# Kernel tuning notes

Measured on AMD Instinct MI355X. Metric: run time of the kernel, lower is better.

The kernel has to match this reference:

```python
import jax, jax.numpy as jnp
import numpy as np

B, S, E, H = 32, 4096, 1024, 16
D = E // H  # head_dim = 64


def setup_inputs() -> dict:
    key = jax.random.key(0)
    ks = jax.random.split(key, 6)
    scale = 1.0 / np.sqrt(E)
    x = jax.random.normal(ks[0], (B, S, E), dtype=jnp.float32)
    mask = jax.random.randint(ks[1], (B, S), 0, 2).astype(bool)  # True = masked key
    in_proj_w = jax.random.uniform(ks[2], (3 * E, E), jnp.float32, -scale, scale)
    in_proj_b = jnp.zeros((3 * E,), jnp.float32)
    out_w = jax.random.uniform(ks[3], (E, E), jnp.float32, -scale, scale)
    out_b = jnp.zeros((E,), jnp.float32)
    return {"x": x, "mask": mask, "in_proj_w": in_proj_w, "in_proj_b": in_proj_b,
            "out_w": out_w, "out_b": out_b}


def reference(x, mask, in_proj_w, in_proj_b, out_w, out_b):
    # nn.MultiheadAttention with q = x[:, 0:1, :], k = v = x, key_padding_mask=mask
    Wq, Wk, Wv = in_proj_w[:E], in_proj_w[E:2 * E], in_proj_w[2 * E:]
    bq, bk, bv = in_proj_b[:E], in_proj_b[E:2 * E], in_proj_b[2 * E:]
    q = (x[:, 0, :] @ Wq.T + bq).reshape(B, H, D)            # (B,H,D)
    k = (x @ Wk.T + bk).reshape(B, S, H, D)                  # (B,S,H,D)
    v = (x @ Wv.T + bv).reshape(B, S, H, D)
    scores = jnp.einsum('bhd,bshd->bhs', q, k) / np.sqrt(D)  # (B,H,S)
    scores = jnp.where(mask[:, None, :], jnp.float32(-1e30), scores)
    attn = jax.nn.softmax(scores, axis=-1)                   # (B,H,S)
    ctx = jnp.einsum('bhs,bshd->bhd', attn, v).reshape(B, E)
    out = ctx @ out_w.T + out_b                              # (B,E) == attn_output.squeeze(1)
    attn_weights = attn.mean(axis=1)[:, None, :]             # (B,1,S): heads averaged
    return out, attn_weights
```

## Files before the change

### kernel.cpp

```cpp
#include <hip/hip_runtime.h>
#include <math.h>


constexpr int cB = 32, cS = 4096, cE = 1024, cH = 16, cD = 64, cNC = 16;

constexpr size_t OFF_P    = 0;
constexpr size_t OFF_C    = OFF_P + 524288;
constexpr size_t OFF_Q    = OFF_C + 512;
constexpr size_t OFF_SC   = OFF_Q + 32768;
constexpr size_t OFF_CTX  = OFF_SC + 2097152;
constexpr size_t OFF_SM   = OFF_CTX + 32768;
constexpr size_t OFF_SL   = OFF_SM + 8192;
constexpr size_t OFF_MF   = OFF_SL + 8192;
constexpr size_t OFF_IL   = OFF_MF + 512;
constexpr size_t OFF_PART = OFF_IL + 512;

__device__ inline float wave_max64(float v) {
#pragma unroll
  for (int m = 1; m < 64; m <<= 1) v = fmaxf(v, __shfl_xor(v, m));
  return v;
}
__device__ inline float wave_sum64(float v) {
#pragma unroll
  for (int m = 1; m < 64; m <<= 1) v += __shfl_xor(v, m);
  return v;
}

__global__ __launch_bounds__(256) void k1a_q(const float* __restrict__ x,
                                             const float* __restrict__ w,
                                             const float* __restrict__ bias,
                                             float* __restrict__ q) {
  int b = blockIdx.x >> 3, blk = blockIdx.x & 7;
  int tid = threadIdx.x;
  __shared__ float x0[cE];
  ((float4*)x0)[tid] = ((const float4*)(x + (size_t)b * cS * cE))[tid];
  __syncthreads();
  int row = blk * 128 + (tid >> 1);
  int half = tid & 1;
  const float* wr = w + (size_t)row * cE + half * 512;
  const float* xl = x0 + half * 512;
  float acc = 0.f;
#pragma unroll 4
  for (int j = 0; j < 128; ++j) {
    float4 a = *(const float4*)(wr + j * 4);
    float4 xv = *(const float4*)(xl + j * 4);
    acc = fmaf(a.x, xv.x, acc); acc = fmaf(a.y, xv.y, acc);
    acc = fmaf(a.z, xv.z, acc); acc = fmaf(a.w, xv.w, acc);
  }
  float tot = acc + __shfl_xor(acc, 1);
  if (!half) q[b * cE + row] = tot + bias[row];
}

__global__ __launch_bounds__(256) void k1b_p(const float* __restrict__ w,
                                             const float* __restrict__ bvec,
                                             const float* __restrict__ q,
                                             float* __restrict__ p,
                                             float* __restrict__ cb) {
  int b = blockIdx.x >> 3, sub = blockIdx.x & 7;
  int ec = sub >> 1, hh = sub & 1;
  int tid = threadIdx.x;
  int e = ec * 256 + tid;
  __shared__ float ql[cE];
  ((float4*)ql)[tid] = ((const float4*)(q + (size_t)b * cE))[tid];
  __syncthreads();
  for (int hi = 0; hi < 8; ++hi) {
    int h = hh * 8 + hi;
    float acc = 0.f;
    const float* wb = w + (size_t)(cE + h * cD) * cE + e;
    const float* qh = ql + h * cD;
#pragma unroll 8
    for (int d = 0; d < cD; ++d) acc = fmaf(wb[(size_t)d * cE], qh[d], acc);
    p[(size_t)(b * cH + h) * cE + e] = 0.125f * acc;
  }
  if (ec == 0 && tid < 8) {
    int h = hh * 8 + tid;
    float cacc = 0.f;
    for (int d = 0; d < cD; ++d) cacc = fmaf(ql[h * cD + d], bvec[cE + h * cD + d], cacc);
    cb[b * cH + h] = 0.125f * cacc;
  }
}

__global__ __launch_bounds__(256) void k2_scores(const float* __restrict__ x,
                                                 const float* __restrict__ p,
                                                 const float* __restrict__ cbias,
                                                 const int* __restrict__ mask,
                                                 float* __restrict__ scores,
                                                 float* __restrict__ statsM,
                                                 float* __restrict__ statsL) {
  __shared__ float xT[2][32 * 256];
  int bx = blockIdx.x;
  int b = bx >> 4, sc = bx & 15;
  int s_base = sc * 256;
  int tid = threadIdx.x;
  int s_t = tid & 63, h_t = tid >> 6;
  int h0 = __builtin_amdgcn_readfirstlane(h_t * 4);
  float acc[4][4];
#pragma unroll
  for (int i = 0; i < 4; ++i)
#pragma unroll
    for (int j = 0; j < 4; ++j) acc[i][j] = 0.f;

  const float* xb = x + ((size_t)b * cS + s_base) * cE;
  const float* __restrict__ pu = p + (size_t)(b * cH + h0) * cE;

  float4 sv[8];
  int r_ = tid >> 3, c4_ = tid & 7;

#pragma unroll
  for (int i = 0; i < 8; ++i)
    sv[i] = *(const float4*)(xb + (size_t)(i * 32 + r_) * cE + c4_ * 4);
  {
    float* xd = xT[0];
#pragma unroll
    for (int i = 0; i < 8; ++i) {
      int r = i * 32 + r_;
      float vv[4] = {sv[i].x, sv[i].y, sv[i].z, sv[i].w};
#pragma unroll
      for (int j = 0; j < 4; ++j) {
        int e = c4_ * 4 + j;
        int f = (e ^ (e >> 4)) & 15;
        xd[e * 256 + ((((r >> 2) ^ f) << 2) | (r & 3))] = vv[j];
      }
    }
  }
  __syncthreads();

  for (int kt = 1; kt <= 32; ++kt) {
    if (kt < 32) {
#pragma unroll
      for (int i = 0; i < 8; ++i)
        sv[i] = *(const float4*)(xb + (size_t)(i * 32 + r_) * cE + kt * 32 + c4_ * 4);
    }
    {
      const float* xs = xT[(kt - 1) & 1];
      const int kb = (kt - 1) * 32;
#pragma unroll 8
      for (int e = 0; e < 32; ++e) {
        int f = (e ^ (e >> 4)) & 15;
        float4 xv = *(const float4*)&xs[e * 256 + ((s_t ^ f) << 2)];
        float p0 = pu[kb + e];
        float p1 = pu[cE + kb + e];
        float p2 = pu[2 * cE + kb + e];
        float p3 = pu[3 * cE + kb + e];
        float xa[4] = {xv.x, xv.y, xv.z, xv.w};
        float pa[4] = {p0, p1, p2, p3};
#pragma unroll
        for (int si = 0; si < 4; ++si)
#pragma unroll
          for (int hj = 0; hj < 4; ++hj) acc[si][hj] = fmaf(xa[si], pa[hj], acc[si][hj]);
      }
    }
    if (kt < 32) {
      float* xd = xT[kt & 1];
#pragma unroll
      for (int i = 0; i < 8; ++i) {
        int r = i * 32 + r_;
        float vv[4] = {sv[i].x, sv[i].y, sv[i].z, sv[i].w};
#pragma unroll
        for (int j = 0; j < 4; ++j) {
          int e = c4_ * 4 + j;
          int f = (e ^ (e >> 4)) & 15;
          xd[e * 256 + ((((r >> 2) ^ f) << 2) | (r & 3))] = vv[j];
        }
      }
    }
    __syncthreads();
  }

  float4 cv = *(const float4*)(cbias + b * cH + h0);
  float ca[4] = {cv.x, cv.y, cv.z, cv.w};
  int4 m4 = *(const int4*)(mask + (size_t)b * cS + s_base + s_t * 4);
#pragma unroll
  for (int hj = 0; hj < 4; ++hj) {
    float v0 = m4.x ? -1e30f : acc[0][hj] + ca[hj];
    float v1 = m4.y ? -1e30f : acc[1][hj] + ca[hj];
    float v2 = m4.z ? -1e30f : acc[2][hj] + ca[hj];
    float v3 = m4.w ? -1e30f : acc[3][hj] + ca[hj];
    *(float4*)(scores + (size_t)(b * cH + h0 + hj) * cS + s_base + s_t * 4) =
        make_float4(v0, v1, v2, v3);
    float mx = fmaxf(fmaxf(v0, v1), fmaxf(v2, v3));
    float wm = wave_max64(mx);
    float es = __expf(v0 - wm) + __expf(v1 - wm) + __expf(v2 - wm) + __expf(v3 - wm);
    float wsum = wave_sum64(es);
    if (s_t == 0) {
      statsM[(size_t)(b * cH + h0 + hj) * cNC + sc] = wm;
      statsL[(size_t)(b * cH + h0 + hj) * cNC + sc] = wsum;
    }
  }
}

__global__ __launch_bounds__(64) void k3t_stats(const float* __restrict__ statsM,
                                                const float* __restrict__ statsL,
                                                float* __restrict__ Mf,
                                                float* __restrict__ iLf) {
  int bh = blockIdx.x * 64 + threadIdx.x;
  const float* sm = statsM + (size_t)bh * cNC;
  const float* sl = statsL + (size_t)bh * cNC;
  float M = -3e38f;
#pragma unroll
  for (int c = 0; c < cNC; ++c) M = fmaxf(M, sm[c]);
  float L = 0.f;
#pragma unroll
  for (int c = 0; c < cNC; ++c) L += sl[c] * __expf(sm[c] - M);
  Mf[bh] = M;
  iLf[bh] = 1.0f / L;
}

__global__ __launch_bounds__(256) void k4_wsum(const float* __restrict__ x,
                                               const float* __restrict__ scores,
                                               const float* __restrict__ Mf,
                                               const float* __restrict__ iLf,
                                               float* __restrict__ part,
                                               float* __restrict__ out) {
  __shared__ float al[2][cH][64];
  int bx = blockIdx.x;
  int b = bx >> 4, sc = bx & 15;
  int tid = threadIdx.x;
  int wv = tid >> 6, lane = tid & 63;
  int e0 = tid * 4;
  const float* xb = x + ((size_t)b * cS + sc * 256) * cE + e0;
  const float* sb = scores + (size_t)b * cH * cS + sc * 256;

  float4 acc[16];
#pragma unroll
  for (int h = 0; h < cH; ++h) acc[h] = make_float4(0.f, 0.f, 0.f, 0.f);

#pragma unroll
  for (int j = 0; j < 4; ++j) {
    int h = wv * 4 + j;
    float Mh = Mf[b * cH + h];
    float iLh = iLf[b * cH + h];
    float v = sb[(size_t)h * cS + lane];
    al[0][h][lane] = __expf(v - Mh) * iLh;
  }
  __syncthreads();

  for (int g = 0; g < 4; ++g) {
    if (g < 3) {
#pragma unroll
      for (int j = 0; j < 4; ++j) {
        int h = wv * 4 + j;
        float Mh = Mf[b * cH + h];
        float iLh = iLf[b * cH + h];
        float v = sb[(size_t)h * cS + (g + 1) * 64 + lane];
        al[(g + 1) & 1][h][lane] = __expf(v - Mh) * iLh;
      }
    }
    const float (*ab)[64] = al[g & 1];
    const float* xg = xb + (size_t)(g * 64) * cE;
#pragma unroll 4
    for (int s = 0; s < 64; ++s) {
      float4 xv = *(const float4*)(xg + (size_t)s * cE);
      float aa[16];
#pragma unroll
      for (int h = 0; h < cH; ++h) aa[h] = ab[h][s];
#pragma unroll
      for (int h = 0; h < cH; ++h) {
        acc[h].x = fmaf(aa[h], xv.x, acc[h].x);
        acc[h].y = fmaf(aa[h], xv.y, acc[h].y);
        acc[h].z = fmaf(aa[h], xv.z, acc[h].z);
        acc[h].w = fmaf(aa[h], xv.w, acc[h].w);
      }
    }
    if (wv == g) {
      float ms = 0.f;
#pragma unroll
      for (int h = 0; h < cH; ++h) ms += ab[h][lane];
      out[cB * cE + (size_t)b * cS + sc * 256 + g * 64 + lane] = ms * (1.0f / 16.0f);
    }
    __syncthreads();
  }

  float* pb = part + ((size_t)(b * cNC + sc) * cH) * cE + e0;
#pragma unroll
  for (int h = 0; h < cH; ++h) *(float4*)(pb + (size_t)h * cE) = acc[h];
}

__global__ __launch_bounds__(256) void k5_ctx(const float* __restrict__ w,
                                              const float* __restrict__ bvec,
                                              const float* __restrict__ part,
                                              float* __restrict__ ctx) {
  int b = blockIdx.x >> 4, h = blockIdx.x & 15;
  int tid = threadIdx.x;
  __shared__ float yl[cE];
  float4 a = make_float4(0.f, 0.f, 0.f, 0.f);
  const float* pb = part + ((size_t)(b * cNC) * cH + h) * cE + tid * 4;
#pragma unroll
  for (int s = 0; s < cNC; ++s) {
    float4 v = *(const float4*)(pb + (size_t)s * cH * cE);
    a.x += v.x; a.y += v.y; a.z += v.z; a.w += v.w;
  }
  *(float4*)(yl + tid * 4) = a;
  __syncthreads();
  int wid = tid >> 6, lane = tid & 63;
  for (int i = 0; i < 16; ++i) {
    int d = wid * 16 + i;
    const float* wr = w + (size_t)(2 * cE + h * cD + d) * cE + lane * 16;
    const float* yr = yl + lane * 16;
    float partial = 0.f;
#pragma unroll
    for (int j = 0; j < 4; ++j) {
      float4 wvv = *(const float4*)(wr + j * 4);
      float4 yv = *(const float4*)(yr + j * 4);
      partial = fmaf(wvv.x, yv.x, partial); partial = fmaf(wvv.y, yv.y, partial);
      partial = fmaf(wvv.z, yv.z, partial); partial = fmaf(wvv.w, yv.w, partial);
    }
    partial = wave_sum64(partial);
    if (lane == 0) ctx[b * cE + h * cD + d] = partial + bvec[2 * cE + h * cD + d];
  }
}

__global__ __launch_bounds__(256) void k6_out(const float* __restrict__ w,
                                              const float* __restrict__ bvec,
                                              const float* __restrict__ ctx,
                                              float* __restrict__ out) {
  int b = blockIdx.x >> 3, br = blockIdx.x & 7;
  int tid = threadIdx.x;
  __shared__ float cl[cE];
  ((float4*)cl)[tid] = ((const float4*)(ctx + (size_t)b * cE))[tid];
  __syncthreads();
  int wid = tid >> 6, lane = tid & 63;
  for (int i = 0; i < 32; ++i) {
    int row = br * 128 + wid * 32 + i;
    const float* wr = w + (size_t)row * cE + lane * 16;
    const float* cr = cl + lane * 16;
    float partial = 0.f;
#pragma unroll
    for (int j = 0; j < 4; ++j) {
      float4 wvv = *(const float4*)(wr + j * 4);
      float4 cvv = *(const float4*)(cr + j * 4);
      partial = fmaf(wvv.x, cvv.x, partial); partial = fmaf(wvv.y, cvv.y, partial);
      partial = fmaf(wvv.z, cvv.z, partial); partial = fmaf(wvv.w, cvv.w, partial);
    }
    partial = wave_sum64(partial);
    if (lane == 0) out[(size_t)b * cE + row] = partial + bvec[row];
  }
}

extern "C" void kernel_launch(void* const* d_in, const int* in_sizes, int n_in,
                              void* d_out, int out_size, void* d_ws, size_t ws_size,
                              hipStream_t stream) {
  const float* x = (const float*)d_in[0];
  const int* mask = (const int*)d_in[1];
  const float* in_proj_w = (const float*)d_in[2];
  const float* in_proj_b = (const float*)d_in[3];
  const float* out_w = (const float*)d_in[4];
  const float* out_b = (const float*)d_in[5];
  float* out = (float*)d_out;
  float* W = (float*)d_ws;

  float* p = W + OFF_P;
  float* cb = W + OFF_C;
  float* q = W + OFF_Q;
  float* scores = W + OFF_SC;
  float* ctx = W + OFF_CTX;
  float* statsM = W + OFF_SM;
  float* statsL = W + OFF_SL;
  float* Mf = W + OFF_MF;
  float* iLf = W + OFF_IL;
  float* part = W + OFF_PART;

  k1a_q<<<256, 256, 0, stream>>>(x, in_proj_w, in_proj_b, q);
  k1b_p<<<256, 256, 0, stream>>>(in_proj_w, in_proj_b, q, p, cb);
  k2_scores<<<512, 256, 0, stream>>>(x, p, cb, mask, scores, statsM, statsL);
  k3t_stats<<<8, 64, 0, stream>>>(statsM, statsL, Mf, iLf);
  k4_wsum<<<512, 256, 0, stream>>>(x, scores, Mf, iLf, part, out);
  k5_ctx<<<512, 256, 0, stream>>>(in_proj_w, in_proj_b, part, ctx);
  k6_out<<<256, 256, 0, stream>>>(out_w, out_b, ctx, out);
}
```

Before: 374.8 us.

## Fuse score computation and weighted V-sum into one online-softmax kernel

Merges the score, stats and weighted-sum kernels into a single pass over x using a running max and sum (flash-style online softmax), so x is read from HBM once instead of twice. Per-chunk partial sums are rescaled and combined in the context kernel, and the head-averaged attention weights move to a separate small kernel that rereads the stored scores. The fused kernel launches only 256 blocks with 256 threads and about 128KB of LDS, so occupancy is low and there are many barriers per 16-row step. Its score dot-product loop also issues a long serial chain of LDS reads.

After: 663.9 us. +77.1%, slower.

```diff
diff --git a/kernel.cpp b/kernel.cpp
--- a/kernel.cpp
+++ b/kernel.cpp
@@ -2,24 +2,21 @@
 #include <math.h>
 
 
-constexpr int cB = 32, cS = 4096, cE = 1024, cH = 16, cD = 64, cNC = 16;
+constexpr int cB = 32, cS = 4096, cE = 1024, cH = 16, cD = 64;
+constexpr int cCK = 8;
+constexpr int cSUB = 32;
 
 constexpr size_t OFF_P    = 0;
 constexpr size_t OFF_C    = OFF_P + 524288;
 constexpr size_t OFF_Q    = OFF_C + 512;
 constexpr size_t OFF_SC   = OFF_Q + 32768;
-constexpr size_t OFF_CTX  = OFF_SC + 2097152;
-constexpr size_t OFF_SM   = OFF_CTX + 32768;
-constexpr size_t OFF_SL   = OFF_SM + 8192;
-constexpr size_t OFF_MF   = OFF_SL + 8192;
+constexpr size_t OFF_SM   = OFF_SC + 2097152;
+constexpr size_t OFF_SL   = OFF_SM + 4096;
+constexpr size_t OFF_MF   = OFF_SL + 4096;
 constexpr size_t OFF_IL   = OFF_MF + 512;
-constexpr size_t OFF_PART = OFF_IL + 512;
-
-__device__ inline float wave_max64(float v) {
-#pragma unroll
-  for (int m = 1; m < 64; m <<= 1) v = fmaxf(v, __shfl_xor(v, m));
-  return v;
-}
+constexpr size_t OFF_CTX  = OFF_IL + 512;
+constexpr size_t OFF_PART = OFF_CTX + 32768;
+
 __device__ inline float wave_sum64(float v) {
 #pragma unroll
   for (int m = 1; m < 64; m <<= 1) v += __shfl_xor(v, m);
@@ -80,180 +77,118 @@
   }
 }
 
-__global__ __launch_bounds__(256) void k2_scores(const float* __restrict__ x,
-                                                 const float* __restrict__ p,
-                                                 const float* __restrict__ cbias,
-                                                 const int* __restrict__ mask,
-                                                 float* __restrict__ scores,
-                                                 float* __restrict__ statsM,
-                                                 float* __restrict__ statsL) {
-  __shared__ float xT[2][32 * 256];
-  int bx = blockIdx.x;
-  int b = bx >> 4, sc = bx & 15;
-  int s_base = sc * 256;
-  int tid = threadIdx.x;
-  int s_t = tid & 63, h_t = tid >> 6;
-  int h0 = __builtin_amdgcn_readfirstlane(h_t * 4);
-  float acc[4][4];
-#pragma unroll
-  for (int i = 0; i < 4; ++i)
-#pragma unroll
-    for (int j = 0; j < 4; ++j) acc[i][j] = 0.f;
-
-  const float* xb = x + ((size_t)b * cS + s_base) * cE;
-  const float* __restrict__ pu = p + (size_t)(b * cH + h0) * cE;
-
-  float4 sv[8];
-  int r_ = tid >> 3, c4_ = tid & 7;
-
-#pragma unroll
-  for (int i = 0; i < 8; ++i)
-    sv[i] = *(const float4*)(xb + (size_t)(i * 32 + r_) * cE + c4_ * 4);
-  {
-    float* xd = xT[0];
-#pragma unroll
-    for (int i = 0; i < 8; ++i) {
-      int r = i * 32 + r_;
-      float vv[4] = {sv[i].x, sv[i].y, sv[i].z, sv[i].w};
-#pragma unroll
-      for (int j = 0; j < 4; ++j) {
-        int e = c4_ * 4 + j;
-        int f = (e ^ (e >> 4)) & 15;
-        xd[e * 256 + ((((r >> 2) ^ f) << 2) | (r & 3))] = vv[j];
-      }
-    }
-  }
-  __syncthreads();
-
-  for (int kt = 1; kt <= 32; ++kt) {
-    if (kt < 32) {
-#pragma unroll
-      for (int i = 0; i < 8; ++i)
-        sv[i] = *(const float4*)(xb + (size_t)(i * 32 + r_) * cE + kt * 32 + c4_ * 4);
-    }
-    {
-      const float* xs = xT[(kt - 1) & 1];
-      const int kb = (kt - 1) * 32;
+__global__ __launch_bounds__(256, 1) void kfuse(const float* __restrict__ x,
+                                                const float* __restrict__ p,
+                                                const float* __restrict__ cb,
+                                                const int* __restrict__ mask,
+                                                float* __restrict__ scores,
+                                                float* __restrict__ statsM,
+                                                float* __restrict__ statsL,
+                                                float* __restrict__ part) {
+  __shared__ __align__(16) float pl[cH * cE];
+  __shared__ __align__(16) float xt[16 * cE];
+  __shared__ __align__(16) float exb[16 * cH];
+  __shared__ __align__(16) float scl[cH];
+  int b = blockIdx.x >> 3, ck = blockIdx.x & 7;
+  int tid = threadIdx.x;
+  int sA = tid & 15, hA = tid >> 4;
+  int s0g = ck * 512;
+
+#pragma unroll
+  for (int j = 0; j < 16; ++j) {
+    int idx4 = j * 256 + tid;
+    ((float4*)pl)[idx4] =
+        *(const float4*)(p + (size_t)(b * cH + (idx4 >> 8)) * cE + (size_t)(idx4 & 255) * 4);
+  }
+  float cbh = cb[b * cH + hA];
+
+  float4 acc[16];
+#pragma unroll
+  for (int h = 0; h < cH; ++h) acc[h] = make_float4(0.f, 0.f, 0.f, 0.f);
+  float m_run = -1e30f, l_run = 0.f;
+
+  const float* xbase = x + ((size_t)b * cS + s0g + (tid >> 4)) * cE + (size_t)(tid & 15) * 4;
+  int sw = tid >> 4;
+  int e4b = tid & 15;
+  float4 rv[16];
+#pragma unroll
+  for (int j = 0; j < 16; ++j) rv[j] = *(const float4*)(xbase + j * 64);
+  __syncthreads();
+
+  float4* xt4 = (float4*)xt;
+  const float4* ph4 = (const float4*)(pl + hA * cE);
+  const float4* exb4 = (const float4*)exb;
+  const float4* scl4 = (const float4*)scl;
+
+  for (int sub = 0; sub < cSUB; ++sub) {
+#pragma unroll
+    for (int j = 0; j < 16; ++j) {
+      int e4 = e4b + 16 * j;
+      xt4[sw * 256 + (e4 ^ sw)] = rv[j];
+    }
+    if (sub < cSUB - 1) {
+      const float* xn = xbase + (size_t)(sub + 1) * 16 * cE;
+#pragma unroll
+      for (int j = 0; j < 16; ++j) rv[j] = *(const float4*)(xn + j * 64);
+    }
+    __syncthreads();
+
+    float d0 = 0.f, d1 = 0.f, d2 = 0.f, d3 = 0.f;
 #pragma unroll 8
-      for (int e = 0; e < 32; ++e) {
-        int f = (e ^ (e >> 4)) & 15;
-        float4 xv = *(const float4*)&xs[e * 256 + ((s_t ^ f) << 2)];
-        float p0 = pu[kb + e];
-        float p1 = pu[cE + kb + e];
-        float p2 = pu[2 * cE + kb + e];
-        float p3 = pu[3 * cE + kb + e];
-        float xa[4] = {xv.x, xv.y, xv.z, xv.w};
-        float pa[4] = {p0, p1, p2, p3};
-#pragma unroll
-        for (int si = 0; si < 4; ++si)
-#pragma unroll
-          for (int hj = 0; hj < 4; ++hj) acc[si][hj] = fmaf(xa[si], pa[hj], acc[si][hj]);
-      }
-    }
-    if (kt < 32) {
-      float* xd = xT[kt & 1];
-#pragma unroll
-      for (int i = 0; i < 8; ++i) {
-        int r = i * 32 + r_;
-        float vv[4] = {sv[i].x, sv[i].y, sv[i].z, sv[i].w};
-#pragma unroll
-        for (int j = 0; j < 4; ++j) {
-          int e = c4_ * 4 + j;
-          int f = (e ^ (e >> 4)) & 15;
-          xd[e * 256 + ((((r >> 2) ^ f) << 2) | (r & 3))] = vv[j];
-        }
-      }
-    }
+    for (int e4 = 0; e4 < 256; e4 += 4) {
+      float4 x0 = xt4[sA * 256 + ((e4 + 0) ^ sA)];
+      float4 p0 = ph4[e4 + 0];
+      d0 = fmaf(x0.x, p0.x, d0); d0 = fmaf(x0.y, p0.y, d0);
+      d0 = fmaf(x0.z, p0.z, d0); d0 = fmaf(x0.w, p0.w, d0);
+      float4 x1 = xt4[sA * 256 + ((e4 + 1) ^ sA)];
+      float4 p1 = ph4[e4 + 1];
+      d1 = fmaf(x1.x, p1.x, d1); d1 = fmaf(x1.y, p1.y, d1);
+      d1 = fmaf(x1.z, p1.z, d1); d1 = fmaf(x1.w, p1.w, d1);
+      float4 x2 = xt4[sA * 256 + ((e4 + 2) ^ sA)];
+      float4 p2 = ph4[e4 + 2];
+      d2 = fmaf(x2.x, p2.x, d2); d2 = fmaf(x2.y, p2.y, d2);
+      d2 = fmaf(x2.z, p2.z, d2); d2 = fmaf(x2.w, p2.w, d2);
+      float4 x3 = xt4[sA * 256 + ((e4 + 3) ^ sA)];
+      float4 p3 = ph4[e4 + 3];
+      d3 = fmaf(x3.x, p3.x, d3); d3 = fmaf(x3.y, p3.y, d3);
+      d3 = fmaf(x3.z, p3.z, d3); d3 = fmaf(x3.w, p3.w, d3);
+    }
+    float score = (d0 + d1) + (d2 + d3) + cbh;
+    int sg = s0g + sub * 16 + sA;
+    if (mask[(size_t)b * cS + sg]) score = -1e30f;
+    scores[(size_t)(b * cH + hA) * cS + sg] = score;
+    float gm = score;
+#pragma unroll
+    for (int m = 1; m < 16; m <<= 1) gm = fmaxf(gm, __shfl_xor(gm, m));
+    float mnew = fmaxf(m_run, gm);
+    float rs = __expf(m_run - mnew);
+    float ex = __expf(score - mnew);
+    float gs = ex;
+#pragma unroll
+    for (int m = 1; m < 16; m <<= 1) gs += __shfl_xor(gs, m);
+    l_run = l_run * rs + gs;
+    m_run = mnew;
+    exb[sA * cH + hA] = ex;
+    if (sA == 0) scl[hA] = rs;
     __syncthreads();
-  }
-
-  float4 cv = *(const float4*)(cbias + b * cH + h0);
-  float ca[4] = {cv.x, cv.y, cv.z, cv.w};
-  int4 m4 = *(const int4*)(mask + (size_t)b * cS + s_base + s_t * 4);
-#pragma unroll
-  for (int hj = 0; hj < 4; ++hj) {
-    float v0 = m4.x ? -1e30f : acc[0][hj] + ca[hj];
-    float v1 = m4.y ? -1e30f : acc[1][hj] + ca[hj];
-    float v2 = m4.z ? -1e30f : acc[2][hj] + ca[hj];
-    float v3 = m4.w ? -1e30f : acc[3][hj] + ca[hj];
-    *(float4*)(scores + (size_t)(b * cH + h0 + hj) * cS + s_base + s_t * 4) =
-        make_float4(v0, v1, v2, v3);
-    float mx = fmaxf(fmaxf(v0, v1), fmaxf(v2, v3));
-    float wm = wave_max64(mx);
-    float es = __expf(v0 - wm) + __expf(v1 - wm) + __expf(v2 - wm) + __expf(v3 - wm);
-    float wsum = wave_sum64(es);
-    if (s_t == 0) {
-      statsM[(size_t)(b * cH + h0 + hj) * cNC + sc] = wm;
-      statsL[(size_t)(b * cH + h0 + hj) * cNC + sc] = wsum;
-    }
-  }
-}
-
-__global__ __launch_bounds__(64) void k3t_stats(const float* __restrict__ statsM,
-                                                const float* __restrict__ statsL,
-                                                float* __restrict__ Mf,
-                                                float* __restrict__ iLf) {
-  int bh = blockIdx.x * 64 + threadIdx.x;
-  const float* sm = statsM + (size_t)bh * cNC;
-  const float* sl = statsL + (size_t)bh * cNC;
-  float M = -3e38f;
-#pragma unroll
-  for (int c = 0; c < cNC; ++c) M = fmaxf(M, sm[c]);
-  float L = 0.f;
-#pragma unroll
-  for (int c = 0; c < cNC; ++c) L += sl[c] * __expf(sm[c] - M);
-  Mf[bh] = M;
-  iLf[bh] = 1.0f / L;
-}
-
-__global__ __launch_bounds__(256) void k4_wsum(const float* __restrict__ x,
-                                               const float* __restrict__ scores,
-                                               const float* __restrict__ Mf,
-                                               const float* __restrict__ iLf,
-                                               float* __restrict__ part,
-                                               float* __restrict__ out) {
-  __shared__ float al[2][cH][64];
-  int bx = blockIdx.x;
-  int b = bx >> 4, sc = bx & 15;
-  int tid = threadIdx.x;
-  int wv = tid >> 6, lane = tid & 63;
-  int e0 = tid * 4;
-  const float* xb = x + ((size_t)b * cS + sc * 256) * cE + e0;
-  const float* sb = scores + (size_t)b * cH * cS + sc * 256;
-
-  float4 acc[16];
-#pragma unroll
-  for (int h = 0; h < cH; ++h) acc[h] = make_float4(0.f, 0.f, 0.f, 0.f);
-
-#pragma unroll
-  for (int j = 0; j < 4; ++j) {
-    int h = wv * 4 + j;
-    float Mh = Mf[b * cH + h];
-    float iLh = iLf[b * cH + h];
-    float v = sb[(size_t)h * cS + lane];
-    al[0][h][lane] = __expf(v - Mh) * iLh;
-  }
-  __syncthreads();
-
-  for (int g = 0; g < 4; ++g) {
-    if (g < 3) {
-#pragma unroll
-      for (int j = 0; j < 4; ++j) {
-        int h = wv * 4 + j;
-        float Mh = Mf[b * cH + h];
-        float iLh = iLf[b * cH + h];
-        float v = sb[(size_t)h * cS + (g + 1) * 64 + lane];
-        al[(g + 1) & 1][h][lane] = __expf(v - Mh) * iLh;
-      }
-    }
-    const float (*ab)[64] = al[g & 1];
-    const float* xg = xb + (size_t)(g * 64) * cE;
+
+#pragma unroll
+    for (int k = 0; k < 4; ++k) {
+      float4 sv = scl4[k];
+      acc[k * 4 + 0].x *= sv.x; acc[k * 4 + 0].y *= sv.x; acc[k * 4 + 0].z *= sv.x; acc[k * 4 + 0].w *= sv.x;
+      acc[k * 4 + 1].x *= sv.y; acc[k * 4 + 1].y *= sv.y; acc[k * 4 + 1].z *= sv.y; acc[k * 4 + 1].w *= sv.y;
+      acc[k * 4 + 2].x *= sv.z; acc[k * 4 + 2].y *= sv.z; acc[k * 4 + 2].z *= sv.z; acc[k * 4 + 2].w *= sv.z;
+      acc[k * 4 + 3].x *= sv.w; acc[k * 4 + 3].y *= sv.w; acc[k * 4 + 3].z *= sv.w; acc[k * 4 + 3].w *= sv.w;
+    }
 #pragma unroll 4
-    for (int s = 0; s < 64; ++s) {
-      float4 xv = *(const float4*)(xg + (size_t)s * cE);
-      float aa[16];
-#pragma unroll
-      for (int h = 0; h < cH; ++h) aa[h] = ab[h][s];
+    for (int s = 0; s < 16; ++s) {
+      float4 xv = xt4[s * 256 + (tid ^ s)];
+      float4 ea = exb4[s * 4 + 0];
+      float4 eb = exb4[s * 4 + 1];
+      float4 ec = exb4[s * 4 + 2];
+      float4 ed = exb4[s * 4 + 3];
+      float aa[16] = {ea.x, ea.y, ea.z, ea.w, eb.x, eb.y, eb.z, eb.w,
+                      ec.x, ec.y, ec.z, ec.w, ed.x, ed.y, ed.z, ed.w};
 #pragma unroll
       for (int h = 0; h < cH; ++h) {
         acc[h].x = fmaf(aa[h], xv.x, acc[h].x);
@@ -262,34 +197,51 @@
         acc[h].w = fmaf(aa[h], xv.w, acc[h].w);
       }
     }
-    if (wv == g) {
-      float ms = 0.f;
-#pragma unroll
-      for (int h = 0; h < cH; ++h) ms += ab[h][lane];
-      out[cB * cE + (size_t)b * cS + sc * 256 + g * 64 + lane] = ms * (1.0f / 16.0f);
-    }
     __syncthreads();
   }
 
-  float* pb = part + ((size_t)(b * cNC + sc) * cH) * cE + e0;
+  float* pb = part + (size_t)(b * cCK + ck) * cH * cE + (size_t)tid * 4;
 #pragma unroll
   for (int h = 0; h < cH; ++h) *(float4*)(pb + (size_t)h * cE) = acc[h];
+  if (sA == 0) {
+    statsM[(b * cH + hA) * cCK + ck] = m_run;
+    statsL[(b * cH + hA) * cCK + ck] = l_run;
+  }
 }
 
 __global__ __launch_bounds__(256) void k5_ctx(const float* __restrict__ w,
                                               const float* __restrict__ bvec,
                                               const float* __restrict__ part,
-                                              float* __restrict__ ctx) {
+                                              const float* __restrict__ statsM,
+                                              const float* __restrict__ statsL,
+                                              float* __restrict__ ctx,
+                                              float* __restrict__ Mf,
+                                              float* __restrict__ iLf) {
   int b = blockIdx.x >> 4, h = blockIdx.x & 15;
+  int bh = b * cH + h;
   int tid = threadIdx.x;
   __shared__ float yl[cE];
+  float M = -3e38f;
+#pragma unroll
+  for (int c = 0; c < cCK; ++c) M = fmaxf(M, statsM[bh * cCK + c]);
+  float L = 0.f;
+  float wgt[cCK];
+#pragma unroll
+  for (int c = 0; c < cCK; ++c) {
+    wgt[c] = __expf(statsM[bh * cCK + c] - M);
+    L += statsL[bh * cCK + c] * wgt[c];
+  }
+  float iL = 1.0f / L;
+  if (blockIdx.x < 512 && tid == 0) { Mf[bh] = M; iLf[bh] = iL; }
   float4 a = make_float4(0.f, 0.f, 0.f, 0.f);
-  const float* pb = part + ((size_t)(b * cNC) * cH + h) * cE + tid * 4;
-#pragma unroll
-  for (int s = 0; s < cNC; ++s) {
-    float4 v = *(const float4*)(pb + (size_t)s * cH * cE);
-    a.x += v.x; a.y += v.y; a.z += v.z; a.w += v.w;
-  }
+  const float* pb = part + (size_t)b * cCK * cH * cE + (size_t)h * cE + (size_t)tid * 4;
+#pragma unroll
+  for (int c = 0; c < cCK; ++c) {
+    float4 v = *(const float4*)(pb + (size_t)c * cH * cE);
+    a.x = fmaf(v.x, wgt[c], a.x); a.y = fmaf(v.y, wgt[c], a.y);
+    a.z = fmaf(v.z, wgt[c], a.z); a.w = fmaf(v.w, wgt[c], a.w);
+  }
+  a.x *= iL; a.y *= iL; a.z *= iL; a.w *= iL;
   *(float4*)(yl + tid * 4) = a;
   __syncthreads();
   int wid = tid >> 6, lane = tid & 63;
@@ -300,14 +252,29 @@
     float partial = 0.f;
 #pragma unroll
     for (int j = 0; j < 4; ++j) {
-      float4 wvv = *(const float4*)(wr + j * 4);
+      float4 wv = *(const float4*)(wr + j * 4);
       float4 yv = *(const float4*)(yr + j * 4);
-      partial = fmaf(wvv.x, yv.x, partial); partial = fmaf(wvv.y, yv.y, partial);
-      partial = fmaf(wvv.z, yv.z, partial); partial = fmaf(wvv.w, yv.w, partial);
+      partial = fmaf(wv.x, yv.x, partial); partial = fmaf(wv.y, yv.y, partial);
+      partial = fmaf(wv.z, yv.z, partial); partial = fmaf(wv.w, yv.w, partial);
     }
     partial = wave_sum64(partial);
     if (lane == 0) ctx[b * cE + h * cD + d] = partial + bvec[2 * cE + h * cD + d];
   }
+}
+
+__global__ __launch_bounds__(256) void kmean(const float* __restrict__ scores,
+                                             const float* __restrict__ Mf,
+                                             const float* __restrict__ iLf,
+                                             float* __restrict__ out) {
+  int idx = blockIdx.x * 256 + threadIdx.x;
+  int b = idx >> 12, s = idx & 4095;
+  float sum = 0.f;
+#pragma unroll
+  for (int h = 0; h < cH; ++h) {
+    float v = scores[(size_t)(b * cH + h) * cS + s];
+    sum += __expf(v - Mf[b * cH + h]) * iLf[b * cH + h];
+  }
+  out[cB * cE + (size_t)b * cS + s] = sum * (1.0f / 16.0f);
 }
 
 __global__ __launch_bounds__(256) void k6_out(const float* __restrict__ w,
@@ -327,10 +294,10 @@
     float partial = 0.f;
 #pragma unroll
     for (int j = 0; j < 4; ++j) {
-      float4 wvv = *(const float4*)(wr + j * 4);
-      float4 cvv = *(const float4*)(cr + j * 4);
-      partial = fmaf(wvv.x, cvv.x, partial); partial = fmaf(wvv.y, cvv.y, partial);
-      partial = fmaf(wvv.z, cvv.z, partial); partial = fmaf(wvv.w, cvv.w, partial);
+      float4 wv = *(const float4*)(wr + j * 4);
+      float4 cv = *(const float4*)(cr + j * 4);
+      partial = fmaf(wv.x, cv.x, partial); partial = fmaf(wv.y, cv.y, partial);
+      partial = fmaf(wv.z, cv.z, partial); partial = fmaf(wv.w, cv.w, partial);
     }
     partial = wave_sum64(partial);
     if (lane == 0) out[(size_t)b * cE + row] = partial + bvec[row];
@@ -353,18 +320,17 @@
   float* cb = W + OFF_C;
   float* q = W + OFF_Q;
   float* scores = W + OFF_SC;
-  float* ctx = W + OFF_CTX;
   float* statsM = W + OFF_SM;
   float* statsL = W + OFF_SL;
   float* Mf = W + OFF_MF;
   float* iLf = W + OFF_IL;
+  float* ctx = W + OFF_CTX;
   float* part = W + OFF_PART;
 
   k1a_q<<<256, 256, 0, stream>>>(x, in_proj_w, in_proj_b, q);
   k1b_p<<<256, 256, 0, stream>>>(in_proj_w, in_proj_b, q, p, cb);
-  k2_scores<<<512, 256, 0, stream>>>(x, p, cb, mask, scores, statsM, statsL);
-  k3t_stats<<<8, 64, 0, stream>>>(statsM, statsL, Mf, iLf);
-  k4_wsum<<<512, 256, 0, stream>>>(x, scores, Mf, iLf, part, out);
-  k5_ctx<<<512, 256, 0, stream>>>(in_proj_w, in_proj_b, part, ctx);
+  kfuse<<<256, 256, 0, stream>>>(x, p, cb, mask, scores, statsM, statsL, part);
+  k5_ctx<<<512, 256, 0, stream>>>(in_proj_w, in_proj_b, part, statsM, statsL, ctx, Mf, iLf);
+  kmean<<<512, 256, 0, stream>>>(scores, Mf, iLf, out);
   k6_out<<<256, 256, 0, stream>>>(out_w, out_b, ctx, out);
 }
```

## Transpose attention weight tile in wsum and batch four rows per Wv block

Applied to the files above, without the earlier changes.

In the weighted-sum kernel the shared softmax-weight tile becomes [s][h] with padding, so each step reads 16 head weights as four float4 loads instead of 16 scalar loads. Per-head max and inverse sum are hoisted out of the loop. The context kernel now processes four batch rows per block, so each Wv row is read once for four batches, with 128 blocks instead of 512. The per-thread full dot product drops the wave reductions but gives fewer blocks, which may lower occupancy.

New measurement: 412.8 us. 10.2% more time.

```diff
diff --git a/kernel.cpp b/kernel.cpp
--- a/kernel.cpp
+++ b/kernel.cpp
@@ -8,12 +8,12 @@
 constexpr size_t OFF_C    = OFF_P + 524288;
 constexpr size_t OFF_Q    = OFF_C + 512;
 constexpr size_t OFF_SC   = OFF_Q + 32768;
-constexpr size_t OFF_CTX  = OFF_SC + 2097152;
-constexpr size_t OFF_SM   = OFF_CTX + 32768;
+constexpr size_t OFF_SM   = OFF_SC + 2097152;
 constexpr size_t OFF_SL   = OFF_SM + 8192;
 constexpr size_t OFF_MF   = OFF_SL + 8192;
 constexpr size_t OFF_IL   = OFF_MF + 512;
-constexpr size_t OFF_PART = OFF_IL + 512;
+constexpr size_t OFF_CTX  = OFF_IL + 512;
+constexpr size_t OFF_PART = OFF_CTX + 32768;
 
 __device__ inline float wave_max64(float v) {
 #pragma unroll
@@ -212,48 +212,49 @@
                                                const float* __restrict__ iLf,
                                                float* __restrict__ part,
                                                float* __restrict__ out) {
-  __shared__ float al[2][cH][64];
+  __shared__ float al[2][64][20];
   int bx = blockIdx.x;
   int b = bx >> 4, sc = bx & 15;
   int tid = threadIdx.x;
   int wv = tid >> 6, lane = tid & 63;
   int e0 = tid * 4;
-  const float* xb = x + ((size_t)b * cS + sc * 256) * cE + e0;
   const float* sb = scores + (size_t)b * cH * cS + sc * 256;
-
+  int h0w = wv * 4;
+  float M4[4], iL4[4];
+#pragma unroll
+  for (int j = 0; j < 4; ++j) {
+    M4[j] = Mf[b * cH + h0w + j];
+    iL4[j] = iLf[b * cH + h0w + j];
+  }
   float4 acc[16];
 #pragma unroll
   for (int h = 0; h < cH; ++h) acc[h] = make_float4(0.f, 0.f, 0.f, 0.f);
 
 #pragma unroll
   for (int j = 0; j < 4; ++j) {
-    int h = wv * 4 + j;
-    float Mh = Mf[b * cH + h];
-    float iLh = iLf[b * cH + h];
-    float v = sb[(size_t)h * cS + lane];
-    al[0][h][lane] = __expf(v - Mh) * iLh;
-  }
-  __syncthreads();
-
+    float v = sb[(size_t)(h0w + j) * cS + lane];
+    al[0][lane][h0w + j] = __expf(v - M4[j]) * iL4[j];
+  }
+  __syncthreads();
+
+  const float* xg = x + ((size_t)b * cS + sc * 256) * cE + e0;
   for (int g = 0; g < 4; ++g) {
+    int buf = g & 1;
     if (g < 3) {
 #pragma unroll
       for (int j = 0; j < 4; ++j) {
-        int h = wv * 4 + j;
-        float Mh = Mf[b * cH + h];
-        float iLh = iLf[b * cH + h];
-        float v = sb[(size_t)h * cS + (g + 1) * 64 + lane];
-        al[(g + 1) & 1][h][lane] = __expf(v - Mh) * iLh;
-      }
-    }
-    const float (*ab)[64] = al[g & 1];
-    const float* xg = xb + (size_t)(g * 64) * cE;
+        float v = sb[(size_t)(h0w + j) * cS + (g + 1) * 64 + lane];
+        al[buf ^ 1][lane][h0w + j] = __expf(v - M4[j]) * iL4[j];
+      }
+    }
+    const float* xs = xg + (size_t)g * 64 * cE;
 #pragma unroll 4
     for (int s = 0; s < 64; ++s) {
-      float4 xv = *(const float4*)(xg + (size_t)s * cE);
-      float aa[16];
-#pragma unroll
-      for (int h = 0; h < cH; ++h) aa[h] = ab[h][s];
+      float4 xv = *(const float4*)(xs + (size_t)s * cE);
+      const float4* ar = (const float4*)al[buf][s];
+      float4 a0 = ar[0], a1 = ar[1], a2 = ar[2], a3 = ar[3];
+      float aa[16] = {a0.x, a0.y, a0.z, a0.w, a1.x, a1.y, a1.z, a1.w,
+                      a2.x, a2.y, a2.z, a2.w, a3.x, a3.y, a3.z, a3.w};
 #pragma unroll
       for (int h = 0; h < cH; ++h) {
         acc[h].x = fmaf(aa[h], xv.x, acc[h].x);
@@ -263,9 +264,10 @@
       }
     }
     if (wv == g) {
-      float ms = 0.f;
-#pragma unroll
-      for (int h = 0; h < cH; ++h) ms += ab[h][lane];
+      const float4* ar = (const float4*)al[buf][lane];
+      float4 a0 = ar[0], a1 = ar[1], a2 = ar[2], a3 = ar[3];
+      float ms = (a0.x + a0.y + a0.z + a0.w) + (a1.x + a1.y + a1.z + a1.w) +
+                 (a2.x + a2.y + a2.z + a2.w) + (a3.x + a3.y + a3.z + a3.w);
       out[cB * cE + (size_t)b * cS + sc * 256 + g * 64 + lane] = ms * (1.0f / 16.0f);
     }
     __syncthreads();
@@ -280,34 +282,40 @@
                                               const float* __restrict__ bvec,
                                               const float* __restrict__ part,
                                               float* __restrict__ ctx) {
-  int b = blockIdx.x >> 4, h = blockIdx.x & 15;
-  int tid = threadIdx.x;
-  __shared__ float yl[cE];
-  float4 a = make_float4(0.f, 0.f, 0.f, 0.f);
-  const float* pb = part + ((size_t)(b * cNC) * cH + h) * cE + tid * 4;
-#pragma unroll
-  for (int s = 0; s < cNC; ++s) {
-    float4 v = *(const float4*)(pb + (size_t)s * cH * cE);
-    a.x += v.x; a.y += v.y; a.z += v.z; a.w += v.w;
-  }
-  *(float4*)(yl + tid * 4) = a;
-  __syncthreads();
-  int wid = tid >> 6, lane = tid & 63;
-  for (int i = 0; i < 16; ++i) {
-    int d = wid * 16 + i;
-    const float* wr = w + (size_t)(2 * cE + h * cD + d) * cE + lane * 16;
-    const float* yr = yl + lane * 16;
-    float partial = 0.f;
-#pragma unroll
-    for (int j = 0; j < 4; ++j) {
-      float4 wvv = *(const float4*)(wr + j * 4);
-      float4 yv = *(const float4*)(yr + j * 4);
-      partial = fmaf(wvv.x, yv.x, partial); partial = fmaf(wvv.y, yv.y, partial);
-      partial = fmaf(wvv.z, yv.z, partial); partial = fmaf(wvv.w, yv.w, partial);
-    }
-    partial = wave_sum64(partial);
-    if (lane == 0) ctx[b * cE + h * cD + d] = partial + bvec[2 * cE + h * cD + d];
-  }
+  int h = blockIdx.x >> 3, bq = blockIdx.x & 7;
+  int b0 = bq * 4;
+  int tid = threadIdx.x;
+  __shared__ float yl[4][1028];
+  int bb = tid >> 6, c4 = tid & 63;
+#pragma unroll
+  for (int j = 0; j < 4; ++j) {
+    int col = j * 64 + c4;
+    float4 a = make_float4(0.f, 0.f, 0.f, 0.f);
+    const float* pb = part + ((size_t)((b0 + bb) * cNC) * cH + h) * cE + (size_t)col * 4;
+#pragma unroll
+    for (int ck = 0; ck < cNC; ++ck) {
+      float4 v = *(const float4*)(pb + (size_t)ck * cH * cE);
+      a.x += v.x; a.y += v.y; a.z += v.z; a.w += v.w;
+    }
+    ((float4*)yl[bb])[col] = a;
+  }
+  __syncthreads();
+  int d = tid >> 2, bi = tid & 3;
+  const float* wr = w + (size_t)(2 * cE + h * cD + d) * cE;
+  const float4* yr = (const float4*)yl[bi];
+  float a0 = 0.f, a1 = 0.f;
+#pragma unroll 4
+  for (int e4 = 0; e4 < 256; e4 += 2) {
+    float4 wv4 = ((const float4*)wr)[e4];
+    float4 yv = yr[e4];
+    a0 = fmaf(wv4.x, yv.x, a0); a0 = fmaf(wv4.y, yv.y, a0);
+    a0 = fmaf(wv4.z, yv.z, a0); a0 = fmaf(wv4.w, yv.w, a0);
+    float4 wv5 = ((const float4*)wr)[e4 + 1];
+    float4 yv5 = yr[e4 + 1];
+    a1 = fmaf(wv5.x, yv5.x, a1); a1 = fmaf(wv5.y, yv5.y, a1);
+    a1 = fmaf(wv5.z, yv5.z, a1); a1 = fmaf(wv5.w, yv5.w, a1);
+  }
+  ctx[(size_t)(b0 + bi) * cE + h * cD + d] = a0 + a1 + bvec[2 * cE + h * cD + d];
 }
 
 __global__ __launch_bounds__(256) void k6_out(const float* __restrict__ w,
@@ -327,10 +335,10 @@
     float partial = 0.f;
 #pragma unroll
     for (int j = 0; j < 4; ++j) {
-      float4 wvv = *(const float4*)(wr + j * 4);
-      float4 cvv = *(const float4*)(cr + j * 4);
-      partial = fmaf(wvv.x, cvv.x, partial); partial = fmaf(wvv.y, cvv.y, partial);
-      partial = fmaf(wvv.z, cvv.z, partial); partial = fmaf(wvv.w, cvv.w, partial);
+      float4 wv = *(const float4*)(wr + j * 4);
+      float4 cv = *(const float4*)(cr + j * 4);
+      partial = fmaf(wv.x, cv.x, partial); partial = fmaf(wv.y, cv.y, partial);
+      partial = fmaf(wv.z, cv.z, partial); partial = fmaf(wv.w, cv.w, partial);
     }
     partial = wave_sum64(partial);
     if (lane == 0) out[(size_t)b * cE + row] = partial + bvec[row];
@@ -353,11 +361,11 @@
   float* cb = W + OFF_C;
   float* q = W + OFF_Q;
   float* scores = W + OFF_SC;
-  float* ctx = W + OFF_CTX;
   float* statsM = W + OFF_SM;
   float* statsL = W + OFF_SL;
   float* Mf = W + OFF_MF;
   float* iLf = W + OFF_IL;
+  float* ctx = W + OFF_CTX;
   float* part = W + OFF_PART;
 
   k1a_q<<<256, 256, 0, stream>>>(x, in_proj_w, in_proj_b, q);
@@ -365,6 +373,6 @@
   k2_scores<<<512, 256, 0, stream>>>(x, p, cb, mask, scores, statsM, statsL);
   k3t_stats<<<8, 64, 0, stream>>>(statsM, statsL, Mf, iLf);
   k4_wsum<<<512, 256, 0, stream>>>(x, scores, Mf, iLf, part, out);
-  k5_ctx<<<512, 256, 0, stream>>>(in_proj_w, in_proj_b, part, ctx);
+  k5_ctx<<<128, 256, 0, stream>>>(in_proj_w, in_proj_b, part, ctx);
   k6_out<<<256, 256, 0, stream>>>(out_w, out_b, ctx, out);
 }
```

## Fuse score and weighted-sum passes with local-max rescaling, split head-mean kernel

Applied to the files above, without the earlier changes.

Merges the score kernel and the weighted-sum kernel so each block reuses its chunk's local softmax numerators (computed against the chunk max) to accumulate partial context. Rescaling by the global max and normalizer moves into the context-reduction kernel, and the stats kernel is removed. A separate small kernel now computes the head-averaged attention weights. The goal is to drop one kernel launch and the dependency on global stats between the passes, and to let the x chunk be read back while still cache-warm. The cost is fewer resident blocks because of the larger LDS footprint and an extra read of the scores.

Result: faster. 345.2 us (-7.9%).

```diff
diff --git a/kernel.cpp b/kernel.cpp
--- a/kernel.cpp
+++ b/kernel.cpp
@@ -8,12 +8,12 @@
 constexpr size_t OFF_C    = OFF_P + 524288;
 constexpr size_t OFF_Q    = OFF_C + 512;
 constexpr size_t OFF_SC   = OFF_Q + 32768;
-constexpr size_t OFF_CTX  = OFF_SC + 2097152;
-constexpr size_t OFF_SM   = OFF_CTX + 32768;
+constexpr size_t OFF_SM   = OFF_SC + 2097152;
 constexpr size_t OFF_SL   = OFF_SM + 8192;
 constexpr size_t OFF_MF   = OFF_SL + 8192;
 constexpr size_t OFF_IL   = OFF_MF + 512;
-constexpr size_t OFF_PART = OFF_IL + 512;
+constexpr size_t OFF_CTX  = OFF_IL + 512;
+constexpr size_t OFF_PART = OFF_CTX + 32768;
 
 __device__ inline float wave_max64(float v) {
 #pragma unroll
@@ -80,14 +80,15 @@
   }
 }
 
-__global__ __launch_bounds__(256) void k2_scores(const float* __restrict__ x,
-                                                 const float* __restrict__ p,
-                                                 const float* __restrict__ cbias,
-                                                 const int* __restrict__ mask,
-                                                 float* __restrict__ scores,
-                                                 float* __restrict__ statsM,
-                                                 float* __restrict__ statsL) {
-  __shared__ float xT[2][32 * 256];
+__global__ __launch_bounds__(256) void kfuse2(const float* __restrict__ x,
+                                              const float* __restrict__ p,
+                                              const float* __restrict__ cbias,
+                                              const int* __restrict__ mask,
+                                              float* __restrict__ scores,
+                                              float* __restrict__ statsM,
+                                              float* __restrict__ statsL,
+                                              float* __restrict__ part) {
+  __shared__ __align__(16) float smem[16384];
   int bx = blockIdx.x;
   int b = bx >> 4, sc = bx & 15;
   int s_base = sc * 256;
@@ -110,7 +111,7 @@
   for (int i = 0; i < 8; ++i)
     sv[i] = *(const float4*)(xb + (size_t)(i * 32 + r_) * cE + c4_ * 4);
   {
-    float* xd = xT[0];
+    float* xd = smem;
 #pragma unroll
     for (int i = 0; i < 8; ++i) {
       int r = i * 32 + r_;
@@ -132,7 +133,7 @@
         sv[i] = *(const float4*)(xb + (size_t)(i * 32 + r_) * cE + kt * 32 + c4_ * 4);
     }
     {
-      const float* xs = xT[(kt - 1) & 1];
+      const float* xs = smem + ((kt - 1) & 1) * 8192;
       const int kb = (kt - 1) * 32;
 #pragma unroll 8
       for (int e = 0; e < 32; ++e) {
@@ -151,7 +152,7 @@
       }
     }
     if (kt < 32) {
-      float* xd = xT[kt & 1];
+      float* xd = smem + (kt & 1) * 8192;
 #pragma unroll
       for (int i = 0; i < 8; ++i) {
         int r = i * 32 + r_;
@@ -167,6 +168,7 @@
     __syncthreads();
   }
 
+  float* al = smem;
   float4 cv = *(const float4*)(cbias + b * cH + h0);
   float ca[4] = {cv.x, cv.y, cv.z, cv.w};
   int4 m4 = *(const int4*)(mask + (size_t)b * cS + s_base + s_t * 4);
@@ -180,116 +182,78 @@
         make_float4(v0, v1, v2, v3);
     float mx = fmaxf(fmaxf(v0, v1), fmaxf(v2, v3));
     float wm = wave_max64(mx);
-    float es = __expf(v0 - wm) + __expf(v1 - wm) + __expf(v2 - wm) + __expf(v3 - wm);
-    float wsum = wave_sum64(es);
+    float e0 = __expf(v0 - wm), e1 = __expf(v1 - wm);
+    float e2 = __expf(v2 - wm), e3 = __expf(v3 - wm);
+    float wsum = wave_sum64(e0 + e1 + e2 + e3);
     if (s_t == 0) {
       statsM[(size_t)(b * cH + h0 + hj) * cNC + sc] = wm;
       statsL[(size_t)(b * cH + h0 + hj) * cNC + sc] = wsum;
     }
-  }
-}
-
-__global__ __launch_bounds__(64) void k3t_stats(const float* __restrict__ statsM,
-                                                const float* __restrict__ statsL,
-                                                float* __restrict__ Mf,
-                                                float* __restrict__ iLf) {
-  int bh = blockIdx.x * 64 + threadIdx.x;
-  const float* sm = statsM + (size_t)bh * cNC;
-  const float* sl = statsL + (size_t)bh * cNC;
-  float M = -3e38f;
-#pragma unroll
-  for (int c = 0; c < cNC; ++c) M = fmaxf(M, sm[c]);
-  float L = 0.f;
-#pragma unroll
-  for (int c = 0; c < cNC; ++c) L += sl[c] * __expf(sm[c] - M);
-  Mf[bh] = M;
-  iLf[bh] = 1.0f / L;
-}
-
-__global__ __launch_bounds__(256) void k4_wsum(const float* __restrict__ x,
-                                               const float* __restrict__ scores,
-                                               const float* __restrict__ Mf,
-                                               const float* __restrict__ iLf,
-                                               float* __restrict__ part,
-                                               float* __restrict__ out) {
-  __shared__ float al[2][cH][64];
-  int bx = blockIdx.x;
-  int b = bx >> 4, sc = bx & 15;
-  int tid = threadIdx.x;
-  int wv = tid >> 6, lane = tid & 63;
-  int e0 = tid * 4;
-  const float* xb = x + ((size_t)b * cS + sc * 256) * cE + e0;
-  const float* sb = scores + (size_t)b * cH * cS + sc * 256;
-
-  float4 acc[16];
-#pragma unroll
-  for (int h = 0; h < cH; ++h) acc[h] = make_float4(0.f, 0.f, 0.f, 0.f);
-
-#pragma unroll
-  for (int j = 0; j < 4; ++j) {
-    int h = wv * 4 + j;
-    float Mh = Mf[b * cH + h];
-    float iLh = iLf[b * cH + h];
-    float v = sb[(size_t)h * cS + lane];
-    al[0][h][lane] = __expf(v - Mh) * iLh;
-  }
-  __syncthreads();
-
-  for (int g = 0; g < 4; ++g) {
-    if (g < 3) {
-#pragma unroll
-      for (int j = 0; j < 4; ++j) {
-        int h = wv * 4 + j;
-        float Mh = Mf[b * cH + h];
-        float iLh = iLf[b * cH + h];
-        float v = sb[(size_t)h * cS + (g + 1) * 64 + lane];
-        al[(g + 1) & 1][h][lane] = __expf(v - Mh) * iLh;
-      }
-    }
-    const float (*ab)[64] = al[g & 1];
-    const float* xg = xb + (size_t)(g * 64) * cE;
+    int sl = s_t * 4;
+    al[(sl + 0) * 20 + h0 + hj] = e0;
+    al[(sl + 1) * 20 + h0 + hj] = e1;
+    al[(sl + 2) * 20 + h0 + hj] = e2;
+    al[(sl + 3) * 20 + h0 + hj] = e3;
+  }
+  __syncthreads();
+
+  float4 acc2[16];
+#pragma unroll
+  for (int h = 0; h < cH; ++h) acc2[h] = make_float4(0.f, 0.f, 0.f, 0.f);
+  const float* xg = xb + (size_t)tid * 4;
 #pragma unroll 4
-    for (int s = 0; s < 64; ++s) {
-      float4 xv = *(const float4*)(xg + (size_t)s * cE);
-      float aa[16];
-#pragma unroll
-      for (int h = 0; h < cH; ++h) aa[h] = ab[h][s];
-#pragma unroll
-      for (int h = 0; h < cH; ++h) {
-        acc[h].x = fmaf(aa[h], xv.x, acc[h].x);
-        acc[h].y = fmaf(aa[h], xv.y, acc[h].y);
-        acc[h].z = fmaf(aa[h], xv.z, acc[h].z);
-        acc[h].w = fmaf(aa[h], xv.w, acc[h].w);
-      }
-    }
-    if (wv == g) {
-      float ms = 0.f;
-#pragma unroll
-      for (int h = 0; h < cH; ++h) ms += ab[h][lane];
-      out[cB * cE + (size_t)b * cS + sc * 256 + g * 64 + lane] = ms * (1.0f / 16.0f);
-    }
-    __syncthreads();
-  }
-
-  float* pb = part + ((size_t)(b * cNC + sc) * cH) * cE + e0;
-#pragma unroll
-  for (int h = 0; h < cH; ++h) *(float4*)(pb + (size_t)h * cE) = acc[h];
+  for (int s = 0; s < 256; ++s) {
+    float4 xv = *(const float4*)(xg + (size_t)s * cE);
+    const float4* ar = (const float4*)(al + s * 20);
+    float4 a0 = ar[0], a1 = ar[1], a2 = ar[2], a3 = ar[3];
+    float aa[16] = {a0.x, a0.y, a0.z, a0.w, a1.x, a1.y, a1.z, a1.w,
+                    a2.x, a2.y, a2.z, a2.w, a3.x, a3.y, a3.z, a3.w};
+#pragma unroll
+    for (int h = 0; h < cH; ++h) {
+      acc2[h].x = fmaf(aa[h], xv.x, acc2[h].x);
+      acc2[h].y = fmaf(aa[h], xv.y, acc2[h].y);
+      acc2[h].z = fmaf(aa[h], xv.z, acc2[h].z);
+      acc2[h].w = fmaf(aa[h], xv.w, acc2[h].w);
+    }
+  }
+  float* pb = part + ((size_t)(b * cNC + sc) * cH) * cE + (size_t)tid * 4;
+#pragma unroll
+  for (int h = 0; h < cH; ++h) *(float4*)(pb + (size_t)h * cE) = acc2[h];
 }
 
 __global__ __launch_bounds__(256) void k5_ctx(const float* __restrict__ w,
                                               const float* __restrict__ bvec,
                                               const float* __restrict__ part,
-                                              float* __restrict__ ctx) {
+                                              const float* __restrict__ statsM,
+                                              const float* __restrict__ statsL,
+                                              float* __restrict__ ctx,
+                                              float* __restrict__ Mf,
+                                              float* __restrict__ iLf) {
   int b = blockIdx.x >> 4, h = blockIdx.x & 15;
+  int bh = b * cH + h;
   int tid = threadIdx.x;
   __shared__ float yl[cE];
+  float M = -3e38f;
+#pragma unroll
+  for (int c = 0; c < cNC; ++c) M = fmaxf(M, statsM[bh * cNC + c]);
+  float L = 0.f;
+  float wgt[cNC];
+#pragma unroll
+  for (int c = 0; c < cNC; ++c) {
+    wgt[c] = __expf(statsM[bh * cNC + c] - M);
+    L += statsL[bh * cNC + c] * wgt[c];
+  }
+  float iL = 1.0f / L;
+  if (tid == 0) { Mf[bh] = M; iLf[bh] = iL; }
   float4 a = make_float4(0.f, 0.f, 0.f, 0.f);
-  const float* pb = part + ((size_t)(b * cNC) * cH + h) * cE + tid * 4;
-#pragma unroll
-  for (int s = 0; s < cNC; ++s) {
-    float4 v = *(const float4*)(pb + (size_t)s * cH * cE);
-    a.x += v.x; a.y += v.y; a.z += v.z; a.w += v.w;
-  }
+  const float* pb = part + (size_t)b * cNC * cH * cE + (size_t)h * cE + (size_t)tid * 4;
+#pragma unroll
+  for (int c = 0; c < cNC; ++c) {
+    float4 v = *(const float4*)(pb + (size_t)c * cH * cE);
+    a.x = fmaf(v.x, wgt[c], a.x); a.y = fmaf(v.y, wgt[c], a.y);
+    a.z = fmaf(v.z, wgt[c], a.z); a.w = fmaf(v.w, wgt[c], a.w);
+  }
+  a.x *= iL; a.y *= iL; a.z *= iL; a.w *= iL;
   *(float4*)(yl + tid * 4) = a;
   __syncthreads();
   int wid = tid >> 6, lane = tid & 63;
@@ -300,14 +264,29 @@
     float partial = 0.f;
 #pragma unroll
     for (int j = 0; j < 4; ++j) {
-      float4 wvv = *(const float4*)(wr + j * 4);
+      float4 wv = *(const float4*)(wr + j * 4);
       float4 yv = *(const float4*)(yr + j * 4);
-      partial = fmaf(wvv.x, yv.x, partial); partial = fmaf(wvv.y, yv.y, partial);
-      partial = fmaf(wvv.z, yv.z, partial); partial = fmaf(wvv.w, yv.w, partial);
+      partial = fmaf(wv.x, yv.x, partial); partial = fmaf(wv.y, yv.y, partial);
+      partial = fmaf(wv.z, yv.z, partial); partial = fmaf(wv.w, yv.w, partial);
     }
     partial = wave_sum64(partial);
     if (lane == 0) ctx[b * cE + h * cD + d] = partial + bvec[2 * cE + h * cD + d];
   }
+}
+
+__global__ __launch_bounds__(256) void kmean(const float* __restrict__ scores,
+                                             const float* __restrict__ Mf,
+                                             const float* __restrict__ iLf,
+                                             float* __restrict__ out) {
+  int idx = blockIdx.x * 256 + threadIdx.x;
+  int b = idx >> 12, s = idx & 4095;
+  float sum = 0.f;
+#pragma unroll
+  for (int h = 0; h < cH; ++h) {
+    float v = scores[(size_t)(b * cH + h) * cS + s];
+    sum += __expf(v - Mf[b * cH + h]) * iLf[b * cH + h];
+  }
+  out[cB * cE + (size_t)b * cS + s] = sum * (1.0f / 16.0f);
 }
 
 __global__ __launch_bounds__(256) void k6_out(const float* __restrict__ w,
@@ -327,10 +306,10 @@
     float partial = 0.f;
 #pragma unroll
     for (int j = 0; j < 4; ++j) {
-      float4 wvv = *(const float4*)(wr + j * 4);
-      float4 cvv = *(const float4*)(cr + j * 4);
-      partial = fmaf(wvv.x, cvv.x, partial); partial = fmaf(wvv.y, cvv.y, partial);
-      partial = fmaf(wvv.z, cvv.z, partial); partial = fmaf(wvv.w, cvv.w, partial);
+      float4 wv = *(const float4*)(wr + j * 4);
+      float4 cv = *(const float4*)(cr + j * 4);
+      partial = fmaf(wv.x, cv.x, partial); partial = fmaf(wv.y, cv.y, partial);
+      partial = fmaf(wv.z, cv.z, partial); partial = fmaf(wv.w, cv.w, partial);
     }
     partial = wave_sum64(partial);
     if (lane == 0) out[(size_t)b * cE + row] = partial + bvec[row];
@@ -353,18 +332,17 @@
   float* cb = W + OFF_C;
   float* q = W + OFF_Q;
   float* scores = W + OFF_SC;
-  float* ctx = W + OFF_CTX;
   float* statsM = W + OFF_SM;
   float* statsL = W + OFF_SL;
   float* Mf = W + OFF_MF;
   float* iLf = W + OFF_IL;
+  float* ctx = W + OFF_CTX;
   float* part = W + OFF_PART;
 
   k1a_q<<<256, 256, 0, stream>>>(x, in_proj_w, in_proj_b, q);
   k1b_p<<<256, 256, 0, stream>>>(in_proj_w, in_proj_b, q, p, cb);
-  k2_scores<<<512, 256, 0, stream>>>(x, p, cb, mask, scores, statsM, statsL);
-  k3t_stats<<<8, 64, 0, stream>>>(statsM, statsL, Mf, iLf);
-  k4_wsum<<<512, 256, 0, stream>>>(x, scores, Mf, iLf, part, out);
-  k5_ctx<<<512, 256, 0, stream>>>(in_proj_w, in_proj_b, part, ctx);
+  kfuse2<<<512, 256, 0, stream>>>(x, p, cb, mask, scores, statsM, statsL, part);
+  k5_ctx<<<512, 256, 0, stream>>>(in_proj_w, in_proj_b, part, statsM, statsL, ctx, Mf, iLf);
+  kmean<<<512, 256, 0, stream>>>(scores, Mf, iLf, out);
   k6_out<<<256, 256, 0, stream>>>(out_w, out_b, ctx, out);
 }
```
